# Kernel tuning notes

Hardware: AMD Instinct MI355X
Metric: run time of the kernel (lower is better)

## Reference

```python
import jax, jax.numpy as jnp
import numpy as np
import math

B, S, DM, H = 4, 2048, 1024, 16
HD = DM // H

def setup_inputs() -> dict:
    key = jax.random.key(0)
    ks = jax.random.split(key, 12)
    def lin(k, din, dout):
        bound = 1.0 / math.sqrt(din)
        kw, kb = jax.random.split(k)
        W = jax.random.uniform(kw, (din, dout), jnp.float32, -bound, bound)
        b = jax.random.uniform(kb, (dout,), jnp.float32, -bound, bound)
        return W, b
    Wq, bq = lin(ks[0], DM, DM)
    Wk, bk = lin(ks[1], DM, DM)
    Wv, bv = lin(ks[2], DM, DM)
    Wo, bo = lin(ks[3], DM, DM)
    return {
        "Q": jax.random.normal(ks[4], (B, S, DM), jnp.float32),
        "K": jax.random.normal(ks[5], (B, S, DM), jnp.float32),
        "V": jax.random.normal(ks[6], (B, S, DM), jnp.float32),
        "mask": jnp.ones((B, S), jnp.int32),
        "Wq": Wq, "bq": bq, "Wk": Wk, "bk": bk,
        "Wv": Wv, "bv": bv, "Wo": Wo, "bo": bo,
    }

def reference(Q, K, V, mask, Wq, bq, Wk, bk, Wv, bv, Wo, bo):
    N, qlen, dm = Q.shape
    klen = K.shape[1]
    q = (Q @ Wq + bq).reshape(N, qlen, H, HD)
    k = (K @ Wk + bk).reshape(N, klen, H, HD)
    v = (V @ Wv + bv).reshape(N, klen, H, HD)
    # scores: [B, q, H, k]
    dot = jnp.einsum('bqhd,bkhd->bqhk', q, k) / math.sqrt(HD)
    # mask is 2-D (N, klen): broadcast as (N, 1, 1, klen); positions where mask==0 are masked
    m = (mask == 0)[:, None, None, :]
    dot = jnp.where(m, -jnp.inf, dot)
    weights = jax.nn.softmax(dot.astype(jnp.float32), axis=-1).astype(dot.dtype)
    out = jnp.einsum('bqhk,bkhd->bqhd', weights, v).reshape(N, qlen, dm)
    return out @ Wo + bo
```

## Files before the change

kernel.cpp:

```cpp
#include <hip/hip_runtime.h>
#include <math.h>

#define B_  4
#define S_  2048
#define DM_ 1024
#define H_  16
#define HD_ 64

typedef float f32x4 __attribute__((ext_vector_type(4)));
typedef short bf16x8 __attribute__((ext_vector_type(8)));

#define MFMA16(a, b, c) __builtin_amdgcn_mfma_f32_16x16x32_bf16((a), (b), (c), 0, 0, 0)

static __device__ __forceinline__ unsigned short f2bf(float f) {
    union { float f; unsigned int i; } c; c.f = f;
    unsigned int u = c.i;
    return (unsigned short)((u + 0x7fffu + ((u >> 16) & 1u)) >> 16);
}
static __device__ __forceinline__ unsigned int f2u(float f) {
    union { float f; unsigned int u; } c; c.f = f; return c.u;
}

static __device__ __forceinline__ void async16(const void* g, void* l) {
    __builtin_amdgcn_global_load_lds(
        (__attribute__((address_space(1))) void*)(void*)g,
        (__attribute__((address_space(3))) void*)l, 16, 0, 0);
}

__global__ __launch_bounds__(256) void cast3_bf16(
    const float* __restrict__ q, const float* __restrict__ k,
    const float* __restrict__ v,
    unsigned short* __restrict__ qo, unsigned short* __restrict__ ko,
    unsigned short* __restrict__ vo) {
    const int z = blockIdx.z;
    const float* in = z == 0 ? q : (z == 1 ? k : v);
    unsigned short* out = z == 0 ? qo : (z == 1 ? ko : vo);
    int idx = (blockIdx.x * 256 + threadIdx.x) * 8;
    float4 a = *(const float4*)(in + idx);
    float4 b = *(const float4*)(in + idx + 4);
    *(ushort4*)(out + idx)     = make_ushort4(f2bf(a.x), f2bf(a.y), f2bf(a.z), f2bf(a.w));
    *(ushort4*)(out + idx + 4) = make_ushort4(f2bf(b.x), f2bf(b.y), f2bf(b.z), f2bf(b.w));
}

__global__ __launch_bounds__(256) void wcast4_t(
    const float* __restrict__ w0, const float* __restrict__ w1,
    const float* __restrict__ w2, const float* __restrict__ w3,
    unsigned short* __restrict__ o0, unsigned short* __restrict__ o1,
    unsigned short* __restrict__ o2, unsigned short* __restrict__ o3) {
    __shared__ float tile[64][65];
    const int z = blockIdx.z;
    const float* W = z == 0 ? w0 : (z == 1 ? w1 : (z == 2 ? w2 : w3));
    unsigned short* Wt = z == 0 ? o0 : (z == 1 ? o1 : (z == 2 ? o2 : o3));
    const int t = threadIdx.x;
    const int k0 = blockIdx.y * 64, n0 = blockIdx.x * 64;
    const int r = t >> 4, c4 = (t & 15) * 4;
    #pragma unroll
    for (int s = 0; s < 4; ++s) {
        float4 f = *(const float4*)(W + (size_t)(k0 + s * 16 + r) * DM_ + n0 + c4);
        tile[s * 16 + r][c4 + 0] = f.x; tile[s * 16 + r][c4 + 1] = f.y;
        tile[s * 16 + r][c4 + 2] = f.z; tile[s * 16 + r][c4 + 3] = f.w;
    }
    __syncthreads();
    #pragma unroll
    for (int s = 0; s < 4; ++s) {
        int n = s * 16 + r;
        ushort4 o = make_ushort4(f2bf(tile[c4 + 0][n]), f2bf(tile[c4 + 1][n]),
                                 f2bf(tile[c4 + 2][n]), f2bf(tile[c4 + 3][n]));
        *(ushort4*)(Wt + (size_t)(n0 + n) * DM_ + k0 + c4) = o;
    }
}

static __device__ __forceinline__ void gemm_body(
    const unsigned short* __restrict__ A,
    const unsigned short* __restrict__ Wt,
    const float* __restrict__ bias,
    void* __restrict__ outp, int mode,
    unsigned short* As, unsigned short* Bs)
{
    const int t = threadIdx.x;
    const int w = t >> 6, l = t & 63;
    const int quad = l >> 4, l16 = l & 15;
    const int wr = w >> 1, wc = w & 1;
    const int m0 = blockIdx.y * 128, n0 = blockIdx.x * 128;

    const int srow8 = l >> 3;
    const int sch   = (l & 7) ^ srow8;
    const unsigned short* ag = A  + (size_t)(m0 + w * 32 + srow8) * DM_ + sch * 8;
    const unsigned short* bg = Wt + (size_t)(n0 + w * 32 + srow8) * DM_ + sch * 8;

    const f32x4 fz = {0.f, 0.f, 0.f, 0.f};
    f32x4 acc[4][4];
    #pragma unroll
    for (int i = 0; i < 4; ++i)
        #pragma unroll
        for (int j = 0; j < 4; ++j) acc[i][j] = fz;

    const int rsw = l16 & 7;
    for (int k0 = 0; k0 < DM_; k0 += 64) {
        __syncthreads();
        #pragma unroll
        for (int s = 0; s < 4; ++s) {
            async16(ag + k0 + (size_t)(s * 8) * DM_, &As[(w * 32 + s * 8) * 64]);
            async16(bg + k0 + (size_t)(s * 8) * DM_, &Bs[(w * 32 + s * 8) * 64]);
        }
        __syncthreads();
        #pragma unroll
        for (int c = 0; c < 2; ++c) {
            const int csw = ((c * 4 + quad) ^ rsw) * 8;
            bf16x8 af[4], bfr[4];
            #pragma unroll
            for (int i = 0; i < 4; ++i)
                af[i] = *(const bf16x8*)&As[(wr * 64 + i * 16 + l16) * 64 + csw];
            #pragma unroll
            for (int j = 0; j < 4; ++j)
                bfr[j] = *(const bf16x8*)&Bs[(wc * 64 + j * 16 + l16) * 64 + csw];
            #pragma unroll
            for (int i = 0; i < 4; ++i)
                #pragma unroll
                for (int j = 0; j < 4; ++j)
                    acc[i][j] = MFMA16(af[i], bfr[j], acc[i][j]);
        }
    }

    float bv[4];
    #pragma unroll
    for (int j = 0; j < 4; ++j) bv[j] = bias[n0 + wc * 64 + j * 16 + l16];

    if (mode == 2) {
        float* out = (float*)outp;
        #pragma unroll
        for (int i = 0; i < 4; ++i)
            #pragma unroll
            for (int j = 0; j < 4; ++j) {
                int col = n0 + wc * 64 + j * 16 + l16;
                #pragma unroll
                for (int r = 0; r < 4; ++r) {
                    int row = m0 + wr * 64 + i * 16 + quad * 4 + r;
                    out[(size_t)row * DM_ + col] = acc[i][j][r] + bv[j];
                }
            }
    } else if (mode == 0) {
        unsigned short* out = (unsigned short*)outp;
        #pragma unroll
        for (int i = 0; i < 4; ++i)
            #pragma unroll
            for (int j = 0; j < 4; ++j) {
                int col = n0 + wc * 64 + j * 16 + l16;
                int h = col >> 6, d = col & 63;
                #pragma unroll
                for (int r = 0; r < 4; ++r) {
                    int row = m0 + wr * 64 + i * 16 + quad * 4 + r;
                    int bb = row >> 11, ss = row & (S_ - 1);
                    out[(((size_t)bb * H_ + h) * S_ + ss) * HD_ + d] =
                        f2bf(acc[i][j][r] + bv[j]);
                }
            }
    } else {
        unsigned short* out = (unsigned short*)outp;
        #pragma unroll
        for (int i = 0; i < 4; ++i)
            #pragma unroll
            for (int j = 0; j < 4; ++j) {
                int col = n0 + wc * 64 + j * 16 + l16;
                int h = col >> 6, d = col & 63;
                int row0 = m0 + wr * 64 + i * 16 + quad * 4;
                int bb = row0 >> 11, ss = row0 & (S_ - 1);
                ushort4 o = make_ushort4(f2bf(acc[i][j][0] + bv[j]),
                                         f2bf(acc[i][j][1] + bv[j]),
                                         f2bf(acc[i][j][2] + bv[j]),
                                         f2bf(acc[i][j][3] + bv[j]));
                *(ushort4*)(out + (((size_t)bb * H_ + h) * HD_ + d) * S_ + ss) = o;
            }
    }
}

__global__ __launch_bounds__(256) void gemm_qkv3(
    const unsigned short* __restrict__ Qc, const unsigned short* __restrict__ Kc,
    const unsigned short* __restrict__ Vc,
    const unsigned short* __restrict__ Wqt, const unsigned short* __restrict__ Wkt,
    const unsigned short* __restrict__ Wvt,
    const float* __restrict__ bq, const float* __restrict__ bk,
    const float* __restrict__ bvp,
    unsigned short* __restrict__ qh, unsigned short* __restrict__ kh,
    unsigned short* __restrict__ vth)
{
    __shared__ unsigned short As[128 * 64];
    __shared__ unsigned short Bs[128 * 64];
    const int z = blockIdx.z;
    const unsigned short* A  = z == 0 ? Qc  : (z == 1 ? Kc  : Vc);
    const unsigned short* Wt = z == 0 ? Wqt : (z == 1 ? Wkt : Wvt);
    const float* bias        = z == 0 ? bq  : (z == 1 ? bk  : bvp);
    void* out                = z == 0 ? (void*)qh : (z == 1 ? (void*)kh : (void*)vth);
    gemm_body(A, Wt, bias, out, z == 2 ? 1 : 0, As, Bs);
}

__global__ __launch_bounds__(256) void gemm_omfma(
    const unsigned short* __restrict__ A, const unsigned short* __restrict__ Wt,
    const float* __restrict__ bias, float* __restrict__ out)
{
    __shared__ unsigned short As[128 * 64];
    __shared__ unsigned short Bs[128 * 64];
    gemm_body(A, Wt, bias, out, 2, As, Bs);
}

__global__ __launch_bounds__(256) void attn_mfma(
    const unsigned short* __restrict__ q,
    const unsigned short* __restrict__ k,
    const unsigned short* __restrict__ vt,
    const int* __restrict__ mask,
    unsigned short* __restrict__ out)
{
    __shared__ unsigned short Qs[128 * 64];
    __shared__ unsigned short Ks[64 * 64];
    __shared__ unsigned short Vs[64 * 64];
    __shared__ unsigned short Ps[4][2][16 * 64];
    __shared__ float msf[64];
    const int t = threadIdx.x;
    const int w = t >> 6, l = t & 63;
    const int quad = l >> 4, l16 = l & 15;
    const int b = blockIdx.z, h = blockIdx.y;
    const int q0 = blockIdx.x * 128;
    const size_t hb = ((size_t)b * H_ + h) * S_;
    const float C_ = 0.18033688011112042f;
    const float NINF = -__builtin_inff();

    const int srow8 = l >> 3;
    const int sch   = (l & 7) ^ srow8;

    const unsigned short* qg = q + (hb + q0) * HD_;
    #pragma unroll
    for (int s = 0; s < 4; ++s) {
        int r0 = w * 32 + s * 8;
        async16(qg + (size_t)(r0 + srow8) * HD_ + sch * 8, &Qs[r0 * 64]);
    }
    __syncthreads();
    bf16x8 qf[2][2];
    #pragma unroll
    for (int g = 0; g < 2; ++g)
        #pragma unroll
        for (int c = 0; c < 2; ++c) {
            int row = w * 32 + g * 16 + l16;
            qf[g][c] = *(const bf16x8*)&Qs[row * 64 + (((c * 4 + quad) ^ (row & 7)) * 8)];
        }

    const f32x4 fz = {0.f, 0.f, 0.f, 0.f};
    f32x4 o[2][4];
    float lr[2] = {0.f, 0.f};
    #pragma unroll
    for (int g = 0; g < 2; ++g)
        #pragma unroll
        for (int jv = 0; jv < 4; ++jv) o[g][jv] = fz;

    const unsigned short* kg0 = k + hb * HD_;
    const unsigned short* vg0 = vt + ((size_t)b * H_ + h) * HD_ * S_;
    const int rsw = l16 & 7;

    for (int kt = 0; kt < S_ / 64; ++kt) {
        __syncthreads();
        #pragma unroll
        for (int s = 0; s < 2; ++s) {
            int r0 = w * 16 + s * 8;
            int rr = r0 + srow8;
            async16(kg0 + (size_t)(kt * 64 + rr) * HD_ + sch * 8, &Ks[r0 * 64]);
            async16(vg0 + (size_t)rr * S_ + kt * 64 + sch * 8, &Vs[r0 * 64]);
        }
        if (t < 64) msf[t] = mask[(size_t)b * S_ + kt * 64 + t] ? 0.f : NINF;
        __syncthreads();

        float madd[4][4];
        #pragma unroll
        for (int kk = 0; kk < 4; ++kk) {
            float4 mv = *(const float4*)&msf[kk * 16 + quad * 4];
            madd[kk][0] = mv.x; madd[kk][1] = mv.y;
            madd[kk][2] = mv.z; madd[kk][3] = mv.w;
        }

        bf16x8 kf[4][2], vfr[4][2];
        #pragma unroll
        for (int kk = 0; kk < 4; ++kk) {
            int row = kk * 16 + l16;
            #pragma unroll
            for (int c = 0; c < 2; ++c)
                kf[kk][c] = *(const bf16x8*)&Ks[row * 64 + (((c * 4 + quad) ^ rsw) * 8)];
        }
        #pragma unroll
        for (int jv = 0; jv < 4; ++jv) {
            int row = jv * 16 + l16;
            #pragma unroll
            for (int c = 0; c < 2; ++c)
                vfr[jv][c] = *(const bf16x8*)&Vs[row * 64 + (((c * 4 + quad) ^ rsw) * 8)];
        }

        #pragma unroll
        for (int g = 0; g < 2; ++g) {
            f32x4 sc[4];
            #pragma unroll
            for (int kk = 0; kk < 4; ++kk) sc[kk] = fz;
            #pragma unroll
            for (int kk = 0; kk < 4; ++kk) {
                sc[kk] = MFMA16(kf[kk][0], qf[g][0], sc[kk]);
                sc[kk] = MFMA16(kf[kk][1], qf[g][1], sc[kk]);
            }
            unsigned short* Pg = &Ps[w][g][0];
            float lacc = 0.f;
            #pragma unroll
            for (int kk = 0; kk < 4; ++kk) {
                int kb = (kk * 2 + (quad >> 1)) ^ rsw;
                #pragma unroll
                for (int rp = 0; rp < 2; ++rp) {
                    float p0 = __builtin_amdgcn_exp2f(
                        fmaf(sc[kk][rp * 2 + 0], C_, madd[kk][rp * 2 + 0]));
                    float p1 = __builtin_amdgcn_exp2f(
                        fmaf(sc[kk][rp * 2 + 1], C_, madd[kk][rp * 2 + 1]));
                    unsigned int pk = __builtin_amdgcn_perm(f2u(p1), f2u(p0), 0x07060302u);
                    lacc += p0 + p1;
                    *(unsigned int*)&Pg[l16 * 64 + kb * 8 + (quad & 1) * 4 + rp * 2] = pk;
                }
            }
            lr[g] += lacc;
            bf16x8 pa0 = *(const bf16x8*)&Pg[l16 * 64 + ((quad ^ rsw) * 8)];
            bf16x8 pa1 = *(const bf16x8*)&Pg[l16 * 64 + (((4 + quad) ^ rsw) * 8)];
            #pragma unroll
            for (int jv = 0; jv < 4; ++jv) {
                o[g][jv] = MFMA16(pa0, vfr[jv][0], o[g][jv]);
                o[g][jv] = MFMA16(pa1, vfr[jv][1], o[g][jv]);
            }
        }
    }
    #pragma unroll
    for (int g = 0; g < 2; ++g) {
        float ls = lr[g];
        ls += __shfl_xor(ls, 16);
        ls += __shfl_xor(ls, 32);
        float inv = 1.0f / ls;
        float invr[4];
        #pragma unroll
        for (int r = 0; r < 4; ++r)
            invr[r] = __shfl(inv, (l & 48) | (quad * 4 + r));
        #pragma unroll
        for (int jv = 0; jv < 4; ++jv) {
            int col = h * HD_ + jv * 16 + l16;
            #pragma unroll
            for (int r = 0; r < 4; ++r) {
                int row = q0 + w * 32 + g * 16 + quad * 4 + r;
                out[((size_t)b * S_ + row) * DM_ + col] = f2bf(o[g][jv][r] * invr[r]);
            }
        }
    }
}

extern "C" void kernel_launch(void* const* d_in, const int* in_sizes, int n_in,
                              void* d_out, int out_size, void* d_ws, size_t ws_size,
                              hipStream_t stream) {
    const float* Q    = (const float*)d_in[0];
    const float* K    = (const float*)d_in[1];
    const float* V    = (const float*)d_in[2];
    const int*   mask = (const int*)d_in[3];
    const float* Wq   = (const float*)d_in[4];
    const float* bq   = (const float*)d_in[5];
    const float* Wk   = (const float*)d_in[6];
    const float* bk   = (const float*)d_in[7];
    const float* Wv   = (const float*)d_in[8];
    const float* bv   = (const float*)d_in[9];
    const float* Wo   = (const float*)d_in[10];
    const float* bo   = (const float*)d_in[11];

    char* ws = (char*)d_ws;
    const size_t MB = 1024 * 1024;
    unsigned short* Qc  = (unsigned short*)(ws);
    unsigned short* Kc  = (unsigned short*)(ws + 16 * MB);
    unsigned short* Vc  = (unsigned short*)(ws + 32 * MB);
    unsigned short* Wqt = (unsigned short*)(ws + 48 * MB);
    unsigned short* Wkt = (unsigned short*)(ws + 50 * MB);
    unsigned short* Wvt = (unsigned short*)(ws + 52 * MB);
    unsigned short* Wot = (unsigned short*)(ws + 54 * MB);
    unsigned short* qh  = (unsigned short*)(ws + 56 * MB);
    unsigned short* kh  = (unsigned short*)(ws + 72 * MB);
    unsigned short* vth = (unsigned short*)(ws + 88 * MB);
    unsigned short* ao  = (unsigned short*)(ws + 104 * MB);

    cast3_bf16<<<dim3(4096, 1, 3), 256, 0, stream>>>(Q, K, V, Qc, Kc, Vc);
    wcast4_t<<<dim3(16, 16, 4), 256, 0, stream>>>(Wq, Wk, Wv, Wo, Wqt, Wkt, Wvt, Wot);
    gemm_qkv3<<<dim3(DM_ / 128, (B_ * S_) / 128, 3), 256, 0, stream>>>(
        Qc, Kc, Vc, Wqt, Wkt, Wvt, bq, bk, bv, qh, kh, vth);
    attn_mfma<<<dim3(S_ / 128, H_, B_), 256, 0, stream>>>(qh, kh, vth, mask, ao);
    gemm_omfma<<<dim3(DM_ / 128, (B_ * S_) / 128), 256, 0, stream>>>(ao, Wot, bo, (float*)d_out);
}
```

Before: 358.7 us.

## Prefetch next K/V/mask tile into registers instead of async LDS loads

Replaces the per-iteration direct global-to-LDS async loads of K, V and the mask with a register-staged software pipeline. The next tile is loaded into registers while the current tile is processed, then written to swizzled LDS at the start of the following iteration. The aim is to hide global load latency behind the MFMA compute of the current tile instead of stalling at the barrier. It costs extra VGPRs, which may lower occupancy. Every wave now writes the mask entries redundantly.

```diff
diff --git a/kernel.cpp b/kernel.cpp
--- a/kernel.cpp
+++ b/kernel.cpp
@@ -233,6 +233,27 @@
         int r0 = w * 32 + s * 8;
         async16(qg + (size_t)(r0 + srow8) * HD_ + sch * 8, &Qs[r0 * 64]);
     }
+
+    const int prow = w * 16 + (l >> 2);
+    const int pc0 = l & 3;
+    const unsigned short* kg0 = k + hb * HD_;
+    const unsigned short* vg0 = vt + ((size_t)b * H_ + h) * HD_ * S_;
+    const unsigned short* kgl = kg0 + (size_t)prow * HD_ + pc0 * 8;
+    const unsigned short* vgl = vg0 + (size_t)prow * S_ + pc0 * 8;
+    const int* mgl = mask + (size_t)b * S_ + l;
+    unsigned short* kdst0 = &Ks[prow * 64 + ((pc0 ^ (prow & 7)) * 8)];
+    unsigned short* kdst1 = &Ks[prow * 64 + (((pc0 + 4) ^ (prow & 7)) * 8)];
+    unsigned short* vdst0 = &Vs[prow * 64 + ((pc0 ^ (prow & 7)) * 8)];
+    unsigned short* vdst1 = &Vs[prow * 64 + (((pc0 + 4) ^ (prow & 7)) * 8)];
+
+    bf16x8 kreg[2], vreg[2];
+    int mreg;
+    kreg[0] = *(const bf16x8*)(kgl);
+    kreg[1] = *(const bf16x8*)(kgl + 32);
+    vreg[0] = *(const bf16x8*)(vgl);
+    vreg[1] = *(const bf16x8*)(vgl + 32);
+    mreg = *mgl;
+
     __syncthreads();
     bf16x8 qf[2][2];
     #pragma unroll
@@ -251,20 +272,25 @@
         #pragma unroll
         for (int jv = 0; jv < 4; ++jv) o[g][jv] = fz;
 
-    const unsigned short* kg0 = k + hb * HD_;
-    const unsigned short* vg0 = vt + ((size_t)b * H_ + h) * HD_ * S_;
     const int rsw = l16 & 7;
 
     for (int kt = 0; kt < S_ / 64; ++kt) {
         __syncthreads();
-        #pragma unroll
-        for (int s = 0; s < 2; ++s) {
-            int r0 = w * 16 + s * 8;
-            int rr = r0 + srow8;
-            async16(kg0 + (size_t)(kt * 64 + rr) * HD_ + sch * 8, &Ks[r0 * 64]);
-            async16(vg0 + (size_t)rr * S_ + kt * 64 + sch * 8, &Vs[r0 * 64]);
-        }
-        if (t < 64) msf[t] = mask[(size_t)b * S_ + kt * 64 + t] ? 0.f : NINF;
+        *(bf16x8*)kdst0 = kreg[0];
+        *(bf16x8*)kdst1 = kreg[1];
+        *(bf16x8*)vdst0 = vreg[0];
+        *(bf16x8*)vdst1 = vreg[1];
+        msf[l] = mreg ? 0.f : NINF;
+        {
+            int ktn = kt + 1 < S_ / 64 ? kt + 1 : kt;
+            const unsigned short* kp = kgl + (size_t)ktn * 64 * HD_;
+            const unsigned short* vp = vgl + ktn * 64;
+            kreg[0] = *(const bf16x8*)(kp);
+            kreg[1] = *(const bf16x8*)(kp + 32);
+            vreg[0] = *(const bf16x8*)(vp);
+            vreg[1] = *(const bf16x8*)(vp + 32);
+            mreg = mgl[ktn * 64];
+        }
         __syncthreads();
 
         float madd[4][4];
```

Measured after the change: 370.6 us. 3.3% more time.
